# Kernel optimization log

Measured on AMD Instinct MI355X. Metric: run time of the kernel, lower is better.

Reference implementation:

```python
import jax, jax.numpy as jnp
import numpy as np

D = 1024
H = 16
DK = D // H
HID = 4096
EPS = 1e-5


def setup_inputs() -> dict:
    key = jax.random.key(0)
    ks = jax.random.split(key, 16)
    B, S = 2, 2048
    sc = lambda fan_in: 1.0 / np.sqrt(fan_in)
    inp = {
        "x": jax.random.normal(ks[0], (B, S, D), jnp.float32),
        "y": jax.random.normal(ks[1], (B, S, D), jnp.float32),
        "mask": jnp.ones((B, 1, 1, S), jnp.int32),
        # attention projections, stored [in, out]
        "Wq": jax.random.normal(ks[2], (D, D), jnp.float32) * sc(D),
        "bq": jnp.zeros((D,), jnp.float32),
        "Wk": jax.random.normal(ks[3], (D, D), jnp.float32) * sc(D),
        "bk": jnp.zeros((D,), jnp.float32),
        "Wv": jax.random.normal(ks[4], (D, D), jnp.float32) * sc(D),
        "bv": jnp.zeros((D,), jnp.float32),
        "Wo": jax.random.normal(ks[5], (D, D), jnp.float32) * sc(D),
        "bo": jnp.zeros((D,), jnp.float32),
        # FFN
        "W1": jax.random.normal(ks[6], (D, HID), jnp.float32) * sc(D),
        "b1": jnp.zeros((HID,), jnp.float32),
        "W2": jax.random.normal(ks[7], (HID, D), jnp.float32) * sc(HID),
        "b2": jnp.zeros((D,), jnp.float32),
        # LayerNorms
        "g1": jnp.ones((D,), jnp.float32),
        "be1": jnp.zeros((D,), jnp.float32),
        "g2": jnp.ones((D,), jnp.float32),
        "be2": jnp.zeros((D,), jnp.float32),
    }
    return inp


def _layer_norm(x, g, b):
    m = jnp.mean(x, axis=-1, keepdims=True)
    v = jnp.mean(jnp.square(x - m), axis=-1, keepdims=True)
    return (x - m) * jax.lax.rsqrt(v + EPS) * g + b


def _split_heads(t):  # [B,S,D] -> [B,H,S,DK]
    B, S, _ = t.shape
    return t.reshape(B, S, H, DK).transpose(0, 2, 1, 3)


def reference(x, y, mask, Wq, bq, Wk, bk, Wv, bv, Wo, bo,
              W1, b1, W2, b2, g1, be1, g2, be2):
    scale = 1.0 / np.sqrt(DK)
    Q = _split_heads(x @ Wq + bq)
    K = _split_heads(y @ Wk + bk)
    V = _split_heads(y @ Wv + bv)
    scores = jnp.einsum("bhqd,bhkd->bhqk", Q, K) * scale  # [B,H,S,S]
    scores = jnp.where(mask == 0, jnp.float32(-1e9), scores)
    probs = jax.nn.softmax(scores, axis=-1)
    attn = jnp.einsum("bhqk,bhkd->bhqd", probs, V)
    B, _, S, _ = attn.shape
    attn = attn.transpose(0, 2, 1, 3).reshape(B, S, D)
    mha_out = attn @ Wo + bo
    x1 = _layer_norm(x + mha_out, g1, be1)
    ff = jax.nn.relu(x1 @ W1 + b1) @ W2 + b2
    return _layer_norm(x1 + ff, g2, be2)
```

## Files before the change

### kernel.cpp

```cpp
#include <hip/hip_runtime.h>

#define S_ 2048
#define D_ 1024
#define B_ 2
#define H_ 16
#define DK_ 64
#define HID_ 4096

typedef unsigned short u16;
typedef __attribute__((ext_vector_type(8))) short short8;
typedef __attribute__((ext_vector_type(4))) float f32x4;

__device__ __forceinline__ float bf2f(u16 u) {
  return __uint_as_float(((unsigned int)u) << 16);
}
__device__ __forceinline__ u16 f2bf(float f) {
  unsigned int x = __float_as_uint(f);
  x += 0x7fff + ((x >> 16) & 1);
  return (u16)(x >> 16);
}
__device__ __forceinline__ unsigned int pk2bf(float lo, float hi) {
  return ((__float_as_uint(lo) + 0x8000u) >> 16) | ((__float_as_uint(hi) + 0x8000u) & 0xffff0000u);
}

__global__ void prep_k(
    const float* __restrict__ Wq, const float* __restrict__ Wk,
    const float* __restrict__ Wv, const float* __restrict__ Wo,
    const float* __restrict__ W1, const float* __restrict__ W2,
    const float* __restrict__ x, const float* __restrict__ y,
    u16* __restrict__ WqT, u16* __restrict__ WkT, u16* __restrict__ WvT,
    u16* __restrict__ WoT, u16* __restrict__ W1T, u16* __restrict__ W2T,
    u16* __restrict__ xb, u16* __restrict__ yb) {
  const int z = blockIdx.z;
  if (z < 6) {
    __shared__ u16 tile[32][33];
    const float* in; u16* outp; int R, C;
    switch (z) {
      case 0: in = Wq; outp = WqT; R = 1024; C = 1024; break;
      case 1: in = Wk; outp = WkT; R = 1024; C = 1024; break;
      case 2: in = Wv; outp = WvT; R = 1024; C = 1024; break;
      case 3: in = Wo; outp = WoT; R = 1024; C = 1024; break;
      case 4: in = W1; outp = W1T; R = 1024; C = 4096; break;
      default: in = W2; outp = W2T; R = 4096; C = 1024; break;
    }
    int c0, r0;
    if (z == 5) { c0 = blockIdx.y * 32; r0 = blockIdx.x * 32; }
    else        { c0 = blockIdx.x * 32; r0 = blockIdx.y * 32; }
    if (c0 >= C || r0 >= R) return;
    const int tx = threadIdx.x, ty = threadIdx.y;
    for (int i = ty; i < 32; i += 8)
      tile[i][tx] = f2bf(in[(long)(r0 + i) * C + c0 + tx]);
    __syncthreads();
    for (int i = ty; i < 32; i += 8)
      outp[(long)(c0 + i) * R + r0 + tx] = tile[tx][i];
  } else {
    const float* in = (z == 6) ? x : y;
    u16* outp = (z == 6) ? xb : yb;
    const int lin = (blockIdx.y * 128 + blockIdx.x) * 256 + threadIdx.y * 32 + threadIdx.x;
    float4 v = ((const float4*)in)[lin];
    ((uint2*)outp)[lin] = make_uint2(pk2bf(v.x, v.y)  , 0);
  }
}

__global__ __launch_bounds__(256) void cvt2_k(const float* __restrict__ x, const float* __restrict__ y,
                                              u16* __restrict__ xb, u16* __restrict__ yb) {
  const int z = blockIdx.y;
  const float* in = z ? y : x;
  u16* outp = z ? yb : xb;
  const int i = blockIdx.x * 256 + threadIdx.x;
  float4 v = ((const float4*)in)[i];
  unsigned int lo = (unsigned int)f2bf(v.x) | ((unsigned int)f2bf(v.y) << 16);
  unsigned int hi = (unsigned int)f2bf(v.z) | ((unsigned int)f2bf(v.w) << 16);
  ((uint2*)outp)[i] = make_uint2(lo, hi);
}

template<int MT, int NT, int OUTF32>
__global__ __launch_bounds__(256) void gemm_bt(
    const u16* __restrict__ A, const u16* __restrict__ Bt,
    const float* __restrict__ bias, void* __restrict__ Cv,
    int K, int lda, int ldb, int ldc,
    long sA, long sB, long sC, int relu) {
  constexpr int BM = MT * 32;
  constexpr int BN = NT * 32;
  __shared__ __align__(16) u16 As[BM * 32];
  __shared__ __align__(16) u16 Bs[BN * 32];
  const int z = blockIdx.z;
  A  += (long)z * sA;
  Bt += (long)z * sB;
  const int tid  = threadIdx.x;
  const int lane = tid & 63, wave = tid >> 6;
  const int quad = lane >> 4, l15 = lane & 15;
  const int wm = wave >> 1, wn = wave & 1;
  const u16* Ab = A  + (long)(blockIdx.y * BM) * lda;
  const u16* Bb = Bt + (long)(blockIdx.x * BN) * ldb;

  f32x4 acc[MT][NT];
#pragma unroll
  for (int i = 0; i < MT; ++i)
#pragma unroll
    for (int j = 0; j < NT; ++j) acc[i][j] = (f32x4){0.f, 0.f, 0.f, 0.f};

  const int r0  = tid >> 2;
  const int kk0 = (tid & 3) * 8;

  for (int kt = 0; kt < K; kt += 32) {
#pragma unroll
    for (int p = 0; p < BM / 64; ++p) {
      __builtin_amdgcn_global_load_lds(
          (const __attribute__((address_space(1))) void*)(Ab + (long)(p * 64 + r0) * lda + kt + kk0),
          (__attribute__((address_space(3))) void*)(&As[p * 2048 + tid * 8]), 16, 0, 0);
    }
#pragma unroll
    for (int p = 0; p < BN / 64; ++p) {
      __builtin_amdgcn_global_load_lds(
          (const __attribute__((address_space(1))) void*)(Bb + (long)(p * 64 + r0) * ldb + kt + kk0),
          (__attribute__((address_space(3))) void*)(&Bs[p * 2048 + tid * 8]), 16, 0, 0);
    }
    __syncthreads();
    short8 af[MT], bfr[NT];
#pragma unroll
    for (int mt = 0; mt < MT; ++mt)
      af[mt] = *(const short8*)&As[(wm * (MT * 16) + mt * 16 + l15) * 32 + quad * 8];
#pragma unroll
    for (int nt = 0; nt < NT; ++nt)
      bfr[nt] = *(const short8*)&Bs[(wn * (NT * 16) + nt * 16 + l15) * 32 + quad * 8];
#pragma unroll
    for (int mt = 0; mt < MT; ++mt)
#pragma unroll
      for (int nt = 0; nt < NT; ++nt)
        acc[mt][nt] = __builtin_amdgcn_mfma_f32_16x16x32_bf16(af[mt], bfr[nt], acc[mt][nt], 0, 0, 0);
    __syncthreads();
  }

#pragma unroll
  for (int nt = 0; nt < NT; ++nt) {
    const int col = blockIdx.x * BN + wn * (NT * 16) + nt * 16 + l15;
    const float bvv = bias ? bias[col] : 0.f;
#pragma unroll
    for (int mt = 0; mt < MT; ++mt) {
#pragma unroll
      for (int r = 0; r < 4; ++r) {
        const int row = blockIdx.y * BM + wm * (MT * 16) + mt * 16 + quad * 4 + r;
        float v = acc[mt][nt][r] + bvv;
        if (relu) v = fmaxf(v, 0.f);
        if (OUTF32) ((float*)Cv)[(long)z * sC + (long)row * ldc + col] = v;
        else        ((u16*)Cv)[(long)z * sC + (long)row * ldc + col] = f2bf(v);
      }
    }
  }
}

__global__ __launch_bounds__(256) void qkv_k(
    const u16* __restrict__ xb, const u16* __restrict__ yb,
    const u16* __restrict__ WqT, const u16* __restrict__ WkT, const u16* __restrict__ WvT,
    const float* __restrict__ bq, const float* __restrict__ bk, const float* __restrict__ bv,
    u16* __restrict__ Q, u16* __restrict__ Kp, u16* __restrict__ Vp) {
  __shared__ __align__(16) u16 As[128 * 32];
  __shared__ __align__(16) u16 Bs[128 * 32];
  const int z = blockIdx.z;
  const u16* A  = (z == 0) ? xb : yb;
  const u16* Bt = (z == 0) ? WqT : (z == 1) ? WkT : WvT;
  const float* bias = (z == 0) ? bq : (z == 1) ? bk : bv;
  u16* C = (z == 0) ? Q : (z == 1) ? Kp : Vp;
  const float sc = (z == 0) ? 0.18033688011112042f : 1.0f;
  const int tid  = threadIdx.x;
  const int lane = tid & 63, wave = tid >> 6;
  const int quad = lane >> 4, l15 = lane & 15;
  const int wm = wave >> 1, wn = wave & 1;
  const u16* Ab = A  + (long)(blockIdx.y * 128) * D_;
  const u16* Bb = Bt + (long)(blockIdx.x * 128) * D_;

  f32x4 acc[4][4];
#pragma unroll
  for (int i = 0; i < 4; ++i)
#pragma unroll
    for (int j = 0; j < 4; ++j) acc[i][j] = (f32x4){0.f, 0.f, 0.f, 0.f};

  const int r0  = tid >> 2;
  const int kk0 = (tid & 3) * 8;

  for (int kt = 0; kt < D_; kt += 32) {
#pragma unroll
    for (int p = 0; p < 2; ++p) {
      __builtin_amdgcn_global_load_lds(
          (const __attribute__((address_space(1))) void*)(Ab + (long)(p * 64 + r0) * D_ + kt + kk0),
          (__attribute__((address_space(3))) void*)(&As[p * 2048 + tid * 8]), 16, 0, 0);
      __builtin_amdgcn_global_load_lds(
          (const __attribute__((address_space(1))) void*)(Bb + (long)(p * 64 + r0) * D_ + kt + kk0),
          (__attribute__((address_space(3))) void*)(&Bs[p * 2048 + tid * 8]), 16, 0, 0);
    }
    __syncthreads();
    short8 af[4], bfr[4];
#pragma unroll
    for (int mt = 0; mt < 4; ++mt)
      af[mt] = *(const short8*)&As[(wm * 64 + mt * 16 + l15) * 32 + quad * 8];
#pragma unroll
    for (int nt = 0; nt < 4; ++nt)
      bfr[nt] = *(const short8*)&Bs[(wn * 64 + nt * 16 + l15) * 32 + quad * 8];
#pragma unroll
    for (int mt = 0; mt < 4; ++mt)
#pragma unroll
      for (int nt = 0; nt < 4; ++nt)
        acc[mt][nt] = __builtin_amdgcn_mfma_f32_16x16x32_bf16(af[mt], bfr[nt], acc[mt][nt], 0, 0, 0);
    __syncthreads();
  }

#pragma unroll
  for (int nt = 0; nt < 4; ++nt) {
    const int col = blockIdx.x * 128 + wn * 64 + nt * 16 + l15;
    const float bvv = bias[col];
#pragma unroll
    for (int mt = 0; mt < 4; ++mt) {
#pragma unroll
      for (int r = 0; r < 4; ++r) {
        const int row = blockIdx.y * 128 + wm * 64 + mt * 16 + quad * 4 + r;
        C[(long)row * D_ + col] = f2bf((acc[mt][nt][r] + bvv) * sc);
      }
    }
  }
}

__global__ void vtrans_k(const u16* __restrict__ V, u16* __restrict__ Vt) {
  __shared__ u16 tile[32][33];
  const int bh = blockIdx.z, b = bh >> 4, h = bh & 15;
  const u16* in = V + (long)b * S_ * D_ + h * DK_;
  u16* outp = Vt + (long)bh * DK_ * S_;
  const int s0 = blockIdx.x * 32, d0 = blockIdx.y * 32;
  const int tx = threadIdx.x, ty = threadIdx.y;
  for (int i = ty; i < 32; i += 8)
    tile[i][tx] = in[(long)(s0 + i) * D_ + d0 + tx];
  __syncthreads();
  for (int i = ty; i < 32; i += 8)
    outp[(long)(d0 + i) * S_ + s0 + tx] = tile[tx][i];
}

__global__ __launch_bounds__(256, 4) void flash_k(
    const u16* __restrict__ Q, const u16* __restrict__ Kp, const u16* __restrict__ Vt,
    const int* __restrict__ mask, u16* __restrict__ ctx) {
  __shared__ __align__(16) u16 sQ[2 * 64 * 32];
  __shared__ __align__(16) u16 sK[2 * 2048];
  __shared__ __align__(16) u16 sV[2 * 2048];
  __shared__ __align__(16) u16 sP[64 * 32];

  const int bh = blockIdx.x, qt = blockIdx.y;
  const int b = bh >> 4, h = bh & 15;
  const int tid = threadIdx.x;
  const int w = tid >> 6, lane = tid & 63;
  const int quad = lane >> 4, l15 = lane & 15;
  const int swz = ((l15 ^ (l15 >> 2)) & 3) << 3;

  const u16* Qg  = Q  + ((long)b * S_ + qt * 64) * D_ + h * DK_;
  const u16* Kg  = Kp + (long)b * S_ * D_ + h * DK_;
  const u16* Vtg = Vt + (long)bh * DK_ * S_;
  const int* maskg = mask + (long)b * S_;
  u16* ctxg = ctx + ((long)b * S_ + qt * 64) * D_ + h * DK_;

  const int krow = tid >> 3, kc = tid & 7;
  const u16* kptr = Kg + (long)krow * D_ + kc * 8;
  const int ksw = (kc >> 2) * 1024 + krow * 32 + (kc & 3) * 8;
  const int vrow = tid >> 2, vc = tid & 3;
  const u16* vptr = Vtg + (long)vrow * S_ + vc * 8;
  const int vsw = vrow * 32 + vc * 8;

  uint4 kreg = *(const uint4*)kptr;
  uint4 vreg = *(const uint4*)vptr;

#pragma unroll
  for (int p = 0; p < 2; ++p) {
    const int idx = p * 256 + tid;
    const int row = idx >> 3, cb = idx & 7;
    uint4 v = *(const uint4*)(Qg + (long)row * D_ + cb * 8);
    *(uint4*)&sQ[(cb >> 2) * 2048 + row * 32 + (cb & 3) * 8] = v;
  }
  *(uint4*)&sK[ksw] = kreg;
  *(uint4*)&sV[vsw] = vreg;
  kreg = *(const uint4*)(kptr + 32 * D_);
  vreg = *(const uint4*)(vptr + 32);
  kptr += 64 * D_;
  vptr += 64;
  __syncthreads();

  short8 qf[2];
#pragma unroll
  for (int kt = 0; kt < 2; ++kt)
    qf[kt] = *(const short8*)&sQ[kt * 2048 + (w * 16 + l15) * 32 + quad * 8];

  float lsum = 0.f;
  f32x4 accO[4];
#pragma unroll
  for (int j = 0; j < 4; ++j) accO[j] = (f32x4){0.f, 0.f, 0.f, 0.f};

  for (int t = 0; t < 64; ++t) {
    if (t) __syncthreads();
    const int buf = (t & 1) ? 2048 : 0;
    const int nbuf = buf ^ 2048;
    if (t < 63) {
      *(uint4*)&sK[nbuf + ksw] = kreg;
      *(uint4*)&sV[nbuf + vsw] = vreg;
      if (t < 62) {
        kreg = *(const uint4*)kptr;
        vreg = *(const uint4*)vptr;
        kptr += 32 * D_;
        vptr += 32;
      }
    }
    const int4 mv0 = *(const int4*)(maskg + t * 32 + quad * 4);
    const int4 mv1 = *(const int4*)(maskg + t * 32 + 16 + quad * 4);

    f32x4 accS[2];
    accS[0] = (f32x4){0.f, 0.f, 0.f, 0.f};
    accS[1] = (f32x4){0.f, 0.f, 0.f, 0.f};
#pragma unroll
    for (int kt = 0; kt < 2; ++kt) {
      short8 kf0 = *(const short8*)&sK[buf + kt * 1024 + l15 * 32 + quad * 8];
      short8 kf1 = *(const short8*)&sK[buf + kt * 1024 + (16 + l15) * 32 + quad * 8];
      accS[0] = __builtin_amdgcn_mfma_f32_16x16x32_bf16(kf0, qf[kt], accS[0], 0, 0, 0);
      accS[1] = __builtin_amdgcn_mfma_f32_16x16x32_bf16(kf1, qf[kt], accS[1], 0, 0, 0);
    }
#pragma unroll
    for (int m = 0; m < 2; ++m) {
      const int4 mv = m ? mv1 : mv0;
      float p0 = mv.x ? __builtin_amdgcn_exp2f(accS[m][0]) : 0.f;
      float p1 = mv.y ? __builtin_amdgcn_exp2f(accS[m][1]) : 0.f;
      float p2 = mv.z ? __builtin_amdgcn_exp2f(accS[m][2]) : 0.f;
      float p3 = mv.w ? __builtin_amdgcn_exp2f(accS[m][3]) : 0.f;
      lsum += (p0 + p1) + (p2 + p3);
      *(uint2*)&sP[(w * 16 + l15) * 32 + ((m * 16 + quad * 4) ^ swz)] =
          make_uint2(pk2bf(p0, p1), pk2bf(p2, p3));
    }
    short8 pf = *(const short8*)&sP[(w * 16 + l15) * 32 + ((quad * 8) ^ swz)];
#pragma unroll
    for (int n = 0; n < 4; ++n) {
      short8 vf = *(const short8*)&sV[buf + (n * 16 + l15) * 32 + quad * 8];
      accO[n] = __builtin_amdgcn_mfma_f32_16x16x32_bf16(pf, vf, accO[n], 0, 0, 0);
    }
  }

  lsum += __shfl_xor(lsum, 16, 64);
  lsum += __shfl_xor(lsum, 32, 64);
  float inv[4];
#pragma unroll
  for (int r = 0; r < 4; ++r)
    inv[r] = 1.f / __shfl(lsum, quad * 4 + r, 64);
#pragma unroll
  for (int n = 0; n < 4; ++n) {
#pragma unroll
    for (int r = 0; r < 4; ++r)
      ctxg[(long)(w * 16 + quad * 4 + r) * D_ + n * 16 + l15] = f2bf(accO[n][r] * inv[r]);
  }
}

__device__ __forceinline__ float block_reduce_sum(float v, float* red) {
#pragma unroll
  for (int off = 32; off; off >>= 1) v += __shfl_down(v, off, 64);
  __syncthreads();
  if ((threadIdx.x & 63) == 0) red[threadIdx.x >> 6] = v;
  __syncthreads();
  return red[0] + red[1] + red[2] + red[3];
}

__global__ __launch_bounds__(256) void addln_fb(const float* __restrict__ A, const u16* __restrict__ Bres,
    const float* __restrict__ g, const float* __restrict__ be, u16* __restrict__ outp) {
  __shared__ float red[4];
  const int row = blockIdx.x, tid = threadIdx.x;
  const float4 av = ((const float4*)(A + (long)row * D_))[tid];
  const uint2 bv2 = ((const uint2*)(Bres + (long)row * D_))[tid];
  float xv[4];
  xv[0] = av.x + bf2f((u16)(bv2.x & 0xffff));
  xv[1] = av.y + bf2f((u16)(bv2.x >> 16));
  xv[2] = av.z + bf2f((u16)(bv2.y & 0xffff));
  xv[3] = av.w + bf2f((u16)(bv2.y >> 16));
  float s  = xv[0] + xv[1] + xv[2] + xv[3];
  float ss = xv[0]*xv[0] + xv[1]*xv[1] + xv[2]*xv[2] + xv[3]*xv[3];
  s  = block_reduce_sum(s, red);
  ss = block_reduce_sum(ss, red);
  const float m   = s * (1.0f / 1024.0f);
  const float var = ss * (1.0f / 1024.0f) - m * m;
  const float rs  = rsqrtf(var + 1e-5f);
  const int c0 = tid * 4;
  float v0 = (xv[0] - m) * rs * g[c0 + 0] + be[c0 + 0];
  float v1 = (xv[1] - m) * rs * g[c0 + 1] + be[c0 + 1];
  float v2 = (xv[2] - m) * rs * g[c0 + 2] + be[c0 + 2];
  float v3 = (xv[3] - m) * rs * g[c0 + 3] + be[c0 + 3];
  unsigned int o01 = (unsigned int)f2bf(v0) | ((unsigned int)f2bf(v1) << 16);
  unsigned int o23 = (unsigned int)f2bf(v2) | ((unsigned int)f2bf(v3) << 16);
  ((uint2*)(outp + (long)row * D_))[tid] = make_uint2(o01, o23);
}

__global__ __launch_bounds__(256) void addln4_bf(const u16* __restrict__ A,
    const float* __restrict__ pK, const float* __restrict__ b2,
    const float* __restrict__ g, const float* __restrict__ be, float* __restrict__ outp) {
  __shared__ float red[4];
  const int row = blockIdx.x, tid = threadIdx.x;
  const uint2 av = ((const uint2*)(A + (long)row * D_))[tid];
  const long stride = (long)4096 * 1024;
  const float4 P0 = ((const float4*)(pK + 0 * stride + (long)row * D_))[tid];
  const float4 P1 = ((const float4*)(pK + 1 * stride + (long)row * D_))[tid];
  const float4 P2 = ((const float4*)(pK + 2 * stride + (long)row * D_))[tid];
  const float4 P3 = ((const float4*)(pK + 3 * stride + (long)row * D_))[tid];
  const int c0 = tid * 4;
  float xv[4];
  xv[0] = bf2f((u16)(av.x & 0xffff)) + ((P0.x + P1.x) + (P2.x + P3.x)) + b2[c0 + 0];
  xv[1] = bf2f((u16)(av.x >> 16))    + ((P0.y + P1.y) + (P2.y + P3.y)) + b2[c0 + 1];
  xv[2] = bf2f((u16)(av.y & 0xffff)) + ((P0.z + P1.z) + (P2.z + P3.z)) + b2[c0 + 2];
  xv[3] = bf2f((u16)(av.y >> 16))    + ((P0.w + P1.w) + (P2.w + P3.w)) + b2[c0 + 3];
  float s  = xv[0] + xv[1] + xv[2] + xv[3];
  float ss = xv[0]*xv[0] + xv[1]*xv[1] + xv[2]*xv[2] + xv[3]*xv[3];
  s  = block_reduce_sum(s, red);
  ss = block_reduce_sum(ss, red);
  const float m   = s * (1.0f / 1024.0f);
  const float var = ss * (1.0f / 1024.0f) - m * m;
  const float rs  = rsqrtf(var + 1e-5f);
  float4 o;
  o.x = (xv[0] - m) * rs * g[c0 + 0] + be[c0 + 0];
  o.y = (xv[1] - m) * rs * g[c0 + 1] + be[c0 + 1];
  o.z = (xv[2] - m) * rs * g[c0 + 2] + be[c0 + 2];
  o.w = (xv[3] - m) * rs * g[c0 + 3] + be[c0 + 3];
  ((float4*)(outp + (long)row * D_))[tid] = o;
}

extern "C" void kernel_launch(void* const* d_in, const int* in_sizes, int n_in,
                              void* d_out, int out_size, void* d_ws, size_t ws_size,
                              hipStream_t stream) {
  const float* x   = (const float*)d_in[0];
  const float* y   = (const float*)d_in[1];
  const int* mask  = (const int*)d_in[2];
  const float* Wq = (const float*)d_in[3];  const float* bq = (const float*)d_in[4];
  const float* Wk = (const float*)d_in[5];  const float* bk = (const float*)d_in[6];
  const float* Wv = (const float*)d_in[7];  const float* bv = (const float*)d_in[8];
  const float* Wo = (const float*)d_in[9];  const float* bo = (const float*)d_in[10];
  const float* W1 = (const float*)d_in[11]; const float* b1 = (const float*)d_in[12];
  const float* W2 = (const float*)d_in[13]; const float* b2 = (const float*)d_in[14];
  const float* g1 = (const float*)d_in[15]; const float* be1 = (const float*)d_in[16];
  const float* g2 = (const float*)d_in[17]; const float* be2 = (const float*)d_in[18];
  float* out = (float*)d_out;

  char* w = (char*)d_ws;
  const size_t MB = 1024 * 1024;
  u16* WqT = (u16*)(w + 0 * MB);
  u16* WkT = (u16*)(w + 2 * MB);
  u16* WvT = (u16*)(w + 4 * MB);
  u16* WoT = (u16*)(w + 6 * MB);
  u16* W1T = (u16*)(w + 8 * MB);
  u16* W2T = (u16*)(w + 16 * MB);
  u16* xb  = (u16*)(w + 24 * MB);
  u16* yb  = (u16*)(w + 32 * MB);
  u16* Q   = (u16*)(w + 40 * MB);
  u16* Kp  = (u16*)(w + 48 * MB);
  u16* Vp  = (u16*)(w + 56 * MB);
  u16* Vt  = (u16*)(w + 64 * MB);
  u16* ctx = (u16*)(w + 72 * MB);
  u16* mha = (u16*)(w + 80 * MB);
  u16* x1  = (u16*)(w + 24 * MB);
  u16* h1  = (u16*)(w + 96 * MB);
  float* pK = (float*)(w + 32 * MB);

  prep_k<<<dim3(128, 32, 6), dim3(32, 8), 0, stream>>>(Wq, Wk, Wv, Wo, W1, W2, x, y,
      WqT, WkT, WvT, WoT, W1T, W2T, xb, yb);
  cvt2_k<<<dim3(4096, 2), 256, 0, stream>>>(x, y, xb, yb);

  qkv_k<<<dim3(8, 32, 3), 256, 0, stream>>>(xb, yb, WqT, WkT, WvT, bq, bk, bv, Q, Kp, Vp);

  vtrans_k<<<dim3(64, 2, 32), dim3(32, 8), 0, stream>>>(Vp, Vt);

  flash_k<<<dim3(32, 32), 256, 0, stream>>>(Q, Kp, Vt, mask, ctx);

  gemm_bt<2, 4, 0><<<dim3(8, 64, 1), 256, 0, stream>>>(ctx, WoT, bo, mha,
      1024, 1024, 1024, 1024, 0, 0, 0, 0);
  addln_fb<<<dim3(4096), 256, 0, stream>>>(x, mha, g1, be1, x1);

  gemm_bt<4, 4, 0><<<dim3(32, 32, 1), 256, 0, stream>>>(x1, W1T, b1, h1,
      1024, 1024, 1024, 4096, 0, 0, 0, 1);
  gemm_bt<4, 4, 1><<<dim3(8, 32, 4), 256, 0, stream>>>(h1, W2T, nullptr, (void*)pK,
      1024, 4096, 4096, 1024, 1024, 1024, (long)4096 * 1024, 0);
  addln4_bf<<<dim3(4096), 256, 0, stream>>>(x1, pK, b2, g2, be2, out);
}
```

Baseline: 442.9 us.

## Double flash query tile, swizzle LDS layout, and use bf16 split-K partials

The flash attention kernel now processes 128 query rows per block (two 16-row fragments per wave), so each K/V tile loaded into LDS is reused twice, and it adopts an XOR-swizzled slot layout for Q/K/V/P. It also gives each wave a private P buffer. The Wo projection becomes a 2-way split-K whose partials are summed in the first add+LayerNorm. The W2 projection drops from a 4-way fp32 split-K to a 2-way split-K with bf16 partials, which cuts partial-sum traffic. The dead x/y conversion branch in prep_k is removed. Risks are higher register pressure in flash_k, fewer attention blocks, and precision loss from storing partial sums in bf16.

Result: faster. 411.9 us (-7.0%).

```diff
diff --git a/kernel.cpp b/kernel.cpp
--- a/kernel.cpp
+++ b/kernel.cpp
@@ -11,6 +11,8 @@
 typedef __attribute__((ext_vector_type(8))) short short8;
 typedef __attribute__((ext_vector_type(4))) float f32x4;
 
+#define SLOT(q16, r16) (((q16) * 16) + ((r16) ^ (q16)))
+
 __device__ __forceinline__ float bf2f(u16 u) {
   return __uint_as_float(((unsigned int)u) << 16);
 }
@@ -27,39 +29,29 @@
     const float* __restrict__ Wq, const float* __restrict__ Wk,
     const float* __restrict__ Wv, const float* __restrict__ Wo,
     const float* __restrict__ W1, const float* __restrict__ W2,
-    const float* __restrict__ x, const float* __restrict__ y,
     u16* __restrict__ WqT, u16* __restrict__ WkT, u16* __restrict__ WvT,
-    u16* __restrict__ WoT, u16* __restrict__ W1T, u16* __restrict__ W2T,
-    u16* __restrict__ xb, u16* __restrict__ yb) {
+    u16* __restrict__ WoT, u16* __restrict__ W1T, u16* __restrict__ W2T) {
   const int z = blockIdx.z;
-  if (z < 6) {
-    __shared__ u16 tile[32][33];
-    const float* in; u16* outp; int R, C;
-    switch (z) {
-      case 0: in = Wq; outp = WqT; R = 1024; C = 1024; break;
-      case 1: in = Wk; outp = WkT; R = 1024; C = 1024; break;
-      case 2: in = Wv; outp = WvT; R = 1024; C = 1024; break;
-      case 3: in = Wo; outp = WoT; R = 1024; C = 1024; break;
-      case 4: in = W1; outp = W1T; R = 1024; C = 4096; break;
-      default: in = W2; outp = W2T; R = 4096; C = 1024; break;
-    }
-    int c0, r0;
-    if (z == 5) { c0 = blockIdx.y * 32; r0 = blockIdx.x * 32; }
-    else        { c0 = blockIdx.x * 32; r0 = blockIdx.y * 32; }
-    if (c0 >= C || r0 >= R) return;
-    const int tx = threadIdx.x, ty = threadIdx.y;
-    for (int i = ty; i < 32; i += 8)
-      tile[i][tx] = f2bf(in[(long)(r0 + i) * C + c0 + tx]);
-    __syncthreads();
-    for (int i = ty; i < 32; i += 8)
-      outp[(long)(c0 + i) * R + r0 + tx] = tile[tx][i];
-  } else {
-    const float* in = (z == 6) ? x : y;
-    u16* outp = (z == 6) ? xb : yb;
-    const int lin = (blockIdx.y * 128 + blockIdx.x) * 256 + threadIdx.y * 32 + threadIdx.x;
-    float4 v = ((const float4*)in)[lin];
-    ((uint2*)outp)[lin] = make_uint2(pk2bf(v.x, v.y)  , 0);
-  }
+  __shared__ u16 tile[32][33];
+  const float* in; u16* outp; int R, C;
+  switch (z) {
+    case 0: in = Wq; outp = WqT; R = 1024; C = 1024; break;
+    case 1: in = Wk; outp = WkT; R = 1024; C = 1024; break;
+    case 2: in = Wv; outp = WvT; R = 1024; C = 1024; break;
+    case 3: in = Wo; outp = WoT; R = 1024; C = 1024; break;
+    case 4: in = W1; outp = W1T; R = 1024; C = 4096; break;
+    default: in = W2; outp = W2T; R = 4096; C = 1024; break;
+  }
+  int c0, r0;
+  if (z == 5) { c0 = blockIdx.y * 32; r0 = blockIdx.x * 32; }
+  else        { c0 = blockIdx.x * 32; r0 = blockIdx.y * 32; }
+  if (c0 >= C || r0 >= R) return;
+  const int tx = threadIdx.x, ty = threadIdx.y;
+  for (int i = ty; i < 32; i += 8)
+    tile[i][tx] = f2bf(in[(long)(r0 + i) * C + c0 + tx]);
+  __syncthreads();
+  for (int i = ty; i < 32; i += 8)
+    outp[(long)(c0 + i) * R + r0 + tx] = tile[tx][i];
 }
 
 __global__ __launch_bounds__(256) void cvt2_k(const float* __restrict__ x, const float* __restrict__ y,
@@ -237,66 +229,70 @@
 __global__ __launch_bounds__(256, 4) void flash_k(
     const u16* __restrict__ Q, const u16* __restrict__ Kp, const u16* __restrict__ Vt,
     const int* __restrict__ mask, u16* __restrict__ ctx) {
-  __shared__ __align__(16) u16 sQ[2 * 64 * 32];
-  __shared__ __align__(16) u16 sK[2 * 2048];
-  __shared__ __align__(16) u16 sV[2 * 2048];
-  __shared__ __align__(16) u16 sP[64 * 32];
+  __shared__ __align__(16) u16 sQ[8192];
+  __shared__ __align__(16) u16 sK[2][2048];
+  __shared__ __align__(16) u16 sV[2][2048];
+  __shared__ __align__(16) u16 sP[4][1024];
 
   const int bh = blockIdx.x, qt = blockIdx.y;
   const int b = bh >> 4, h = bh & 15;
   const int tid = threadIdx.x;
   const int w = tid >> 6, lane = tid & 63;
   const int quad = lane >> 4, l15 = lane & 15;
-  const int swz = ((l15 ^ (l15 >> 2)) & 3) << 3;
-
-  const u16* Qg  = Q  + ((long)b * S_ + qt * 64) * D_ + h * DK_;
+
+  const u16* Qg  = Q  + ((long)b * S_ + qt * 128) * D_ + h * DK_;
   const u16* Kg  = Kp + (long)b * S_ * D_ + h * DK_;
   const u16* Vtg = Vt + (long)bh * DK_ * S_;
   const int* maskg = mask + (long)b * S_;
-  u16* ctxg = ctx + ((long)b * S_ + qt * 64) * D_ + h * DK_;
+  u16* ctxg = ctx + ((long)b * S_ + qt * 128) * D_ + h * DK_;
 
   const int krow = tid >> 3, kc = tid & 7;
   const u16* kptr = Kg + (long)krow * D_ + kc * 8;
-  const int ksw = (kc >> 2) * 1024 + krow * 32 + (kc & 3) * 8;
+  const int ksw = (((krow >> 4) * 2 + (kc >> 2)) * 64 + SLOT(kc & 3, krow & 15)) * 8;
   const int vrow = tid >> 2, vc = tid & 3;
   const u16* vptr = Vtg + (long)vrow * S_ + vc * 8;
-  const int vsw = vrow * 32 + vc * 8;
+  const int vsw = ((vrow >> 4) * 64 + SLOT(vc, vrow & 15)) * 8;
 
   uint4 kreg = *(const uint4*)kptr;
   uint4 vreg = *(const uint4*)vptr;
 
 #pragma unroll
-  for (int p = 0; p < 2; ++p) {
+  for (int p = 0; p < 4; ++p) {
     const int idx = p * 256 + tid;
     const int row = idx >> 3, cb = idx & 7;
     uint4 v = *(const uint4*)(Qg + (long)row * D_ + cb * 8);
-    *(uint4*)&sQ[(cb >> 2) * 2048 + row * 32 + (cb & 3) * 8] = v;
-  }
-  *(uint4*)&sK[ksw] = kreg;
-  *(uint4*)&sV[vsw] = vreg;
+    *(uint4*)&sQ[(((row >> 4) * 2 + (cb >> 2)) * 64 + SLOT(cb & 3, row & 15)) * 8] = v;
+  }
+  *(uint4*)&sK[0][ksw] = kreg;
+  *(uint4*)&sV[0][vsw] = vreg;
   kreg = *(const uint4*)(kptr + 32 * D_);
   vreg = *(const uint4*)(vptr + 32);
   kptr += 64 * D_;
   vptr += 64;
   __syncthreads();
 
-  short8 qf[2];
-#pragma unroll
-  for (int kt = 0; kt < 2; ++kt)
-    qf[kt] = *(const short8*)&sQ[kt * 2048 + (w * 16 + l15) * 32 + quad * 8];
-
-  float lsum = 0.f;
-  f32x4 accO[4];
-#pragma unroll
-  for (int j = 0; j < 4; ++j) accO[j] = (f32x4){0.f, 0.f, 0.f, 0.f};
+  const int rslot = SLOT(quad, l15) * 8;
+
+  short8 qf[2][2];
+#pragma unroll
+  for (int mf = 0; mf < 2; ++mf)
+#pragma unroll
+    for (int kt = 0; kt < 2; ++kt)
+      qf[mf][kt] = *(const short8*)&sQ[(((w * 2 + mf) * 2 + kt) * 64) * 8 + rslot];
+
+  float lsum[2] = {0.f, 0.f};
+  f32x4 accO[2][4];
+#pragma unroll
+  for (int i = 0; i < 2; ++i)
+#pragma unroll
+    for (int j = 0; j < 4; ++j) accO[i][j] = (f32x4){0.f, 0.f, 0.f, 0.f};
 
   for (int t = 0; t < 64; ++t) {
     if (t) __syncthreads();
-    const int buf = (t & 1) ? 2048 : 0;
-    const int nbuf = buf ^ 2048;
+    const int buf = t & 1, nb = buf ^ 1;
     if (t < 63) {
-      *(uint4*)&sK[nbuf + ksw] = kreg;
-      *(uint4*)&sV[nbuf + vsw] = vreg;
+      *(uint4*)&sK[nb][ksw] = kreg;
+      *(uint4*)&sV[nb][vsw] = vreg;
       if (t < 62) {
         kreg = *(const uint4*)kptr;
         vreg = *(const uint4*)vptr;
@@ -304,49 +300,67 @@
         vptr += 32;
       }
     }
+    f32x4 accS[2][2];
+#pragma unroll
+    for (int i = 0; i < 2; ++i)
+#pragma unroll
+      for (int j = 0; j < 2; ++j) accS[i][j] = (f32x4){0.f, 0.f, 0.f, 0.f};
+#pragma unroll
+    for (int kt = 0; kt < 2; ++kt) {
+      short8 kf0 = *(const short8*)&sK[buf][(kt * 64) * 8 + rslot];
+      short8 kf1 = *(const short8*)&sK[buf][((2 + kt) * 64) * 8 + rslot];
+#pragma unroll
+      for (int mf = 0; mf < 2; ++mf) {
+        accS[0][mf] = __builtin_amdgcn_mfma_f32_16x16x32_bf16(kf0, qf[mf][kt], accS[0][mf], 0, 0, 0);
+        accS[1][mf] = __builtin_amdgcn_mfma_f32_16x16x32_bf16(kf1, qf[mf][kt], accS[1][mf], 0, 0, 0);
+      }
+    }
     const int4 mv0 = *(const int4*)(maskg + t * 32 + quad * 4);
     const int4 mv1 = *(const int4*)(maskg + t * 32 + 16 + quad * 4);
-
-    f32x4 accS[2];
-    accS[0] = (f32x4){0.f, 0.f, 0.f, 0.f};
-    accS[1] = (f32x4){0.f, 0.f, 0.f, 0.f};
-#pragma unroll
-    for (int kt = 0; kt < 2; ++kt) {
-      short8 kf0 = *(const short8*)&sK[buf + kt * 1024 + l15 * 32 + quad * 8];
-      short8 kf1 = *(const short8*)&sK[buf + kt * 1024 + (16 + l15) * 32 + quad * 8];
-      accS[0] = __builtin_amdgcn_mfma_f32_16x16x32_bf16(kf0, qf[kt], accS[0], 0, 0, 0);
-      accS[1] = __builtin_amdgcn_mfma_f32_16x16x32_bf16(kf1, qf[kt], accS[1], 0, 0, 0);
-    }
-#pragma unroll
-    for (int m = 0; m < 2; ++m) {
-      const int4 mv = m ? mv1 : mv0;
-      float p0 = mv.x ? __builtin_amdgcn_exp2f(accS[m][0]) : 0.f;
-      float p1 = mv.y ? __builtin_amdgcn_exp2f(accS[m][1]) : 0.f;
-      float p2 = mv.z ? __builtin_amdgcn_exp2f(accS[m][2]) : 0.f;
-      float p3 = mv.w ? __builtin_amdgcn_exp2f(accS[m][3]) : 0.f;
-      lsum += (p0 + p1) + (p2 + p3);
-      *(uint2*)&sP[(w * 16 + l15) * 32 + ((m * 16 + quad * 4) ^ swz)] =
-          make_uint2(pk2bf(p0, p1), pk2bf(p2, p3));
-    }
-    short8 pf = *(const short8*)&sP[(w * 16 + l15) * 32 + ((quad * 8) ^ swz)];
+#pragma unroll
+    for (int mk = 0; mk < 2; ++mk) {
+      const int4 mv = mk ? mv1 : mv0;
+      const int qt2 = mk * 2 + (quad >> 1);
+      const int j0 = (quad & 1) * 4;
+#pragma unroll
+      for (int mf = 0; mf < 2; ++mf) {
+        float p0 = mv.x ? __builtin_amdgcn_exp2f(accS[mk][mf][0]) : 0.f;
+        float p1 = mv.y ? __builtin_amdgcn_exp2f(accS[mk][mf][1]) : 0.f;
+        float p2 = mv.z ? __builtin_amdgcn_exp2f(accS[mk][mf][2]) : 0.f;
+        float p3 = mv.w ? __builtin_amdgcn_exp2f(accS[mk][mf][3]) : 0.f;
+        lsum[mf] += (p0 + p1) + (p2 + p3);
+        *(uint2*)&sP[w][(mf * 64 + SLOT(qt2, l15)) * 8 + j0] =
+            make_uint2(pk2bf(p0, p1), pk2bf(p2, p3));
+      }
+    }
+    short8 pf0 = *(const short8*)&sP[w][0 + rslot];
+    short8 pf1 = *(const short8*)&sP[w][64 * 8 + rslot];
 #pragma unroll
     for (int n = 0; n < 4; ++n) {
-      short8 vf = *(const short8*)&sV[buf + (n * 16 + l15) * 32 + quad * 8];
-      accO[n] = __builtin_amdgcn_mfma_f32_16x16x32_bf16(pf, vf, accO[n], 0, 0, 0);
-    }
-  }
-
-  lsum += __shfl_xor(lsum, 16, 64);
-  lsum += __shfl_xor(lsum, 32, 64);
-  float inv[4];
-#pragma unroll
-  for (int r = 0; r < 4; ++r)
-    inv[r] = 1.f / __shfl(lsum, quad * 4 + r, 64);
-#pragma unroll
-  for (int n = 0; n < 4; ++n) {
+      short8 vf = *(const short8*)&sV[buf][(n * 64) * 8 + rslot];
+      accO[0][n] = __builtin_amdgcn_mfma_f32_16x16x32_bf16(pf0, vf, accO[0][n], 0, 0, 0);
+      accO[1][n] = __builtin_amdgcn_mfma_f32_16x16x32_bf16(pf1, vf, accO[1][n], 0, 0, 0);
+    }
+  }
+
+#pragma unroll
+  for (int mf = 0; mf < 2; ++mf) {
+    lsum[mf] += __shfl_xor(lsum[mf], 16, 64);
+    lsum[mf] += __shfl_xor(lsum[mf], 32, 64);
+  }
+#pragma unroll
+  for (int mf = 0; mf < 2; ++mf) {
+    float inv[4];
 #pragma unroll
     for (int r = 0; r < 4; ++r)
-      ctxg[(long)(w * 16 + quad * 4 + r) * D_ + n * 16 + l15] = f2bf(accO[n][r] * inv[r]);
+      inv[r] = 1.f / __shfl(lsum[mf], quad * 4 + r, 64);
+#pragma unroll
+    for (int n = 0; n < 4; ++n) {
+#pragma unroll
+      for (int r = 0; r < 4; ++r)
+        ctxg[(long)(w * 32 + mf * 16 + quad * 4 + r) * D_ + n * 16 + l15] =
+            f2bf(accO[mf][n][r] * inv[r]);
+    }
   }
 }
 
@@ -359,17 +373,20 @@
   return red[0] + red[1] + red[2] + red[3];
 }
 
-__global__ __launch_bounds__(256) void addln_fb(const float* __restrict__ A, const u16* __restrict__ Bres,
+__global__ __launch_bounds__(256) void addln_fb(const float* __restrict__ A,
+    const u16* __restrict__ M0, const u16* __restrict__ M1, const float* __restrict__ bo,
     const float* __restrict__ g, const float* __restrict__ be, u16* __restrict__ outp) {
   __shared__ float red[4];
   const int row = blockIdx.x, tid = threadIdx.x;
   const float4 av = ((const float4*)(A + (long)row * D_))[tid];
-  const uint2 bv2 = ((const uint2*)(Bres + (long)row * D_))[tid];
+  const uint2 m0 = ((const uint2*)(M0 + (long)row * D_))[tid];
+  const uint2 m1 = ((const uint2*)(M1 + (long)row * D_))[tid];
+  const int c0 = tid * 4;
   float xv[4];
-  xv[0] = av.x + bf2f((u16)(bv2.x & 0xffff));
-  xv[1] = av.y + bf2f((u16)(bv2.x >> 16));
-  xv[2] = av.z + bf2f((u16)(bv2.y & 0xffff));
-  xv[3] = av.w + bf2f((u16)(bv2.y >> 16));
+  xv[0] = av.x + bf2f((u16)(m0.x & 0xffff)) + bf2f((u16)(m1.x & 0xffff)) + bo[c0 + 0];
+  xv[1] = av.y + bf2f((u16)(m0.x >> 16))    + bf2f((u16)(m1.x >> 16))    + bo[c0 + 1];
+  xv[2] = av.z + bf2f((u16)(m0.y & 0xffff)) + bf2f((u16)(m1.y & 0xffff)) + bo[c0 + 2];
+  xv[3] = av.w + bf2f((u16)(m0.y >> 16))    + bf2f((u16)(m1.y >> 16))    + bo[c0 + 3];
   float s  = xv[0] + xv[1] + xv[2] + xv[3];
   float ss = xv[0]*xv[0] + xv[1]*xv[1] + xv[2]*xv[2] + xv[3]*xv[3];
   s  = block_reduce_sum(s, red);
@@ -377,7 +394,6 @@
   const float m   = s * (1.0f / 1024.0f);
   const float var = ss * (1.0f / 1024.0f) - m * m;
   const float rs  = rsqrtf(var + 1e-5f);
-  const int c0 = tid * 4;
   float v0 = (xv[0] - m) * rs * g[c0 + 0] + be[c0 + 0];
   float v1 = (xv[1] - m) * rs * g[c0 + 1] + be[c0 + 1];
   float v2 = (xv[2] - m) * rs * g[c0 + 2] + be[c0 + 2];
@@ -387,23 +403,20 @@
   ((uint2*)(outp + (long)row * D_))[tid] = make_uint2(o01, o23);
 }
 
-__global__ __launch_bounds__(256) void addln4_bf(const u16* __restrict__ A,
-    const float* __restrict__ pK, const float* __restrict__ b2,
+__global__ __launch_bounds__(256) void addln2_bf(const u16* __restrict__ A,
+    const u16* __restrict__ F0, const u16* __restrict__ F1, const float* __restrict__ b2,
     const float* __restrict__ g, const float* __restrict__ be, float* __restrict__ outp) {
   __shared__ float red[4];
   const int row = blockIdx.x, tid = threadIdx.x;
   const uint2 av = ((const uint2*)(A + (long)row * D_))[tid];
-  const long stride = (long)4096 * 1024;
-  const float4 P0 = ((const float4*)(pK + 0 * stride + (long)row * D_))[tid];
-  const float4 P1 = ((const float4*)(pK + 1 * stride + (long)row * D_))[tid];
-  const float4 P2 = ((const float4*)(pK + 2 * stride + (long)row * D_))[tid];
-  const float4 P3 = ((const float4*)(pK + 3 * stride + (long)row * D_))[tid];
+  const uint2 f0 = ((const uint2*)(F0 + (long)row * D_))[tid];
+  const uint2 f1 = ((const uint2*)(F1 + (long)row * D_))[tid];
   const int c0 = tid * 4;
   float xv[4];
-  xv[0] = bf2f((u16)(av.x & 0xffff)) + ((P0.x + P1.x) + (P2.x + P3.x)) + b2[c0 + 0];
-  xv[1] = bf2f((u16)(av.x >> 16))    + ((P0.y + P1.y) + (P2.y + P3.y)) + b2[c0 + 1];
-  xv[2] = bf2f((u16)(av.y & 0xffff)) + ((P0.z + P1.z) + (P2.z + P3.z)) + b2[c0 + 2];
-  xv[3] = bf2f((u16)(av.y >> 16))    + ((P0.w + P1.w) + (P2.w + P3.w)) + b2[c0 + 3];
+  xv[0] = bf2f((u16)(av.x & 0xffff)) + bf2f((u16)(f0.x & 0xffff)) + bf2f((u16)(f1.x & 0xffff)) + b2[c0 + 0];
+  xv[1] = bf2f((u16)(av.x >> 16))    + bf2f((u16)(f0.x >> 16))    + bf2f((u16)(f1.x >> 16))    + b2[c0 + 1];
+  xv[2] = bf2f((u16)(av.y & 0xffff)) + bf2f((u16)(f0.y & 0xffff)) + bf2f((u16)(f1.y & 0xffff)) + b2[c0 + 2];
+  xv[3] = bf2f((u16)(av.y >> 16))    + bf2f((u16)(f0.y >> 16))    + bf2f((u16)(f1.y >> 16))    + b2[c0 + 3];
   float s  = xv[0] + xv[1] + xv[2] + xv[3];
   float ss = xv[0]*xv[0] + xv[1]*xv[1] + xv[2]*xv[2] + xv[3]*xv[3];
   s  = block_reduce_sum(s, red);
@@ -453,25 +466,25 @@
   u16* mha = (u16*)(w + 80 * MB);
   u16* x1  = (u16*)(w + 24 * MB);
   u16* h1  = (u16*)(w + 96 * MB);
-  float* pK = (float*)(w + 32 * MB);
-
-  prep_k<<<dim3(128, 32, 6), dim3(32, 8), 0, stream>>>(Wq, Wk, Wv, Wo, W1, W2, x, y,
-      WqT, WkT, WvT, WoT, W1T, W2T, xb, yb);
+  u16* ff  = (u16*)(w + 40 * MB);
+
+  prep_k<<<dim3(128, 32, 6), dim3(32, 8), 0, stream>>>(Wq, Wk, Wv, Wo, W1, W2,
+      WqT, WkT, WvT, WoT, W1T, W2T);
   cvt2_k<<<dim3(4096, 2), 256, 0, stream>>>(x, y, xb, yb);
 
   qkv_k<<<dim3(8, 32, 3), 256, 0, stream>>>(xb, yb, WqT, WkT, WvT, bq, bk, bv, Q, Kp, Vp);
 
   vtrans_k<<<dim3(64, 2, 32), dim3(32, 8), 0, stream>>>(Vp, Vt);
 
-  flash_k<<<dim3(32, 32), 256, 0, stream>>>(Q, Kp, Vt, mask, ctx);
-
-  gemm_bt<2, 4, 0><<<dim3(8, 64, 1), 256, 0, stream>>>(ctx, WoT, bo, mha,
-      1024, 1024, 1024, 1024, 0, 0, 0, 0);
-  addln_fb<<<dim3(4096), 256, 0, stream>>>(x, mha, g1, be1, x1);
+  flash_k<<<dim3(32, 16), 256, 0, stream>>>(Q, Kp, Vt, mask, ctx);
+
+  gemm_bt<4, 4, 0><<<dim3(8, 32, 2), 256, 0, stream>>>(ctx, WoT, nullptr, mha,
+      512, 1024, 1024, 1024, 512, 512, (long)4096 * 1024, 0);
+  addln_fb<<<dim3(4096), 256, 0, stream>>>(x, mha, mha + (long)4096 * 1024, bo, g1, be1, x1);
 
   gemm_bt<4, 4, 0><<<dim3(32, 32, 1), 256, 0, stream>>>(x1, W1T, b1, h1,
       1024, 1024, 1024, 4096, 0, 0, 0, 1);
-  gemm_bt<4, 4, 1><<<dim3(8, 32, 4), 256, 0, stream>>>(h1, W2T, nullptr, (void*)pK,
-      1024, 4096, 4096, 1024, 1024, 1024, (long)4096 * 1024, 0);
-  addln4_bf<<<dim3(4096), 256, 0, stream>>>(x1, pK, b2, g2, be2, out);
-}
+  gemm_bt<4, 4, 0><<<dim3(8, 32, 2), 256, 0, stream>>>(h1, W2T, nullptr, ff,
+      2048, 4096, 4096, 1024, 2048, 2048, (long)4096 * 1024, 0);
+  addln2_bf<<<dim3(4096), 256, 0, stream>>>(x1, ff, ff + (long)4096 * 1024, b2, g2, be2, out);
+}
```
